# Kernel tuning notes

Measured on AMD Instinct MI355X. Metric: run time of the kernel, lower is better.

The kernel has to match this reference:

```python
import jax, jax.numpy as jnp
import numpy as np

NU, NB, NI = 50000, 20000, 100000
D = 64
NUM_LAYERS = 2
CORE_K = 3
PAD = NI  # padding index for bundle_items
BATCH, NCAND = 2048, 2
MAXDEG = 50
E_UB, E_UI, E_BI = 800000, 1000000, 1200000
N_UB, N_UI, N_BI = NU + NB, NU + NI, NB + NI


def setup_inputs():
    key = jax.random.key(0)
    ks = jax.random.split(key, 24)
    f = jnp.float32
    inp = {
        'users_feature': jax.random.normal(ks[0], (NU, D), f) * 0.1,
        'bundles_feature': jax.random.normal(ks[1], (NB, D), f) * 0.1,
        'items_feature': jax.random.normal(ks[2], (NI, D), f) * 0.1,
        'mlp_core_w1': jax.random.normal(ks[3], (2, 32), f) * 0.1,
        'mlp_core_b1': jnp.zeros((32,), f),
        'mlp_core_w2': jax.random.normal(ks[4], (32, 1), f) * 0.1,
        'mlp_core_b2': jnp.zeros((1,), f),
        'mlp_syn_w1': jax.random.normal(ks[5], (2 * D, D), f) * 0.05,
        'mlp_syn_b1': jnp.zeros((D,), f),
        'mlp_syn_w2': jax.random.normal(ks[6], (D, D), f) * 0.05,
        'mlp_syn_b2': jnp.zeros((D,), f),
        'ub_val': jax.random.uniform(ks[7], (E_UB,), f) * 0.2,
        'ui_val': jax.random.uniform(ks[8], (E_UI,), f) * 0.2,
        'bi_val': jax.random.uniform(ks[9], (E_BI,), f) * 0.2,
        'users': jax.random.randint(ks[10], (BATCH,), 0, NU),
        'bundles': jax.random.randint(ks[11], (BATCH, NCAND), 0, NB),
        'ub_row': jax.random.randint(ks[12], (E_UB,), 0, N_UB, jnp.int32),
        'ub_col': jax.random.randint(ks[13], (E_UB,), 0, N_UB, jnp.int32),
        'ui_row': jax.random.randint(ks[14], (E_UI,), 0, N_UI, jnp.int32),
        'ui_col': jax.random.randint(ks[15], (E_UI,), 0, N_UI, jnp.int32),
        'bi_row': jax.random.randint(ks[16], (E_BI,), 0, N_BI, jnp.int32),
        'bi_col': jax.random.randint(ks[17], (E_BI,), 0, N_BI, jnp.int32),
        'bundle_items': jax.random.randint(ks[18], (NB, MAXDEG), 0, NI + 1),
    }
    return inp


def spmm(row, col, val, x):
    # y = A @ x for COO sparse A: gather source rows, scale, scatter-add to dest rows
    return jax.ops.segment_sum(val[:, None] * x[col], row, num_segments=x.shape[0])


def propagate(row, col, val, feat_a, feat_b):
    f = jnp.concatenate([feat_a, feat_b], axis=0)
    acc = f
    for _ in range(NUM_LAYERS):
        f = spmm(row, col, val, f)
        acc = acc + f
    m = acc / (NUM_LAYERS + 1)  # mean over hop outputs
    return m[:feat_a.shape[0]], m[feat_a.shape[0]:]


def core_fringe_scores(users, bundles, reps, bundle_items,
                       cw1, cb1, cw2, cb2, sw1, sb1, sw2, sb2):
    UB_u, UB_b, UI_u, UI_i, BI_b, BI_i = reps
    B, C = bundles.shape
    users_exp = jnp.repeat(users, C)            # [B*C]
    bundles_flat = bundles.reshape(-1)          # [B*C]
    bbi = bundle_items[bundles_flat]            # [B*C, M]
    mask = bbi != PAD
    zero = jnp.zeros((1, D), UI_i.dtype)
    items_ui = jnp.concatenate([UI_i, zero], 0)[bbi]  # [B*C, M, D]
    items_bi = jnp.concatenate([BI_i, zero], 0)[bbi]
    u_ui = UI_u[users_exp]                      # [B*C, D]
    b_bi = BI_b[bundles_flat]
    r_UI = jnp.einsum('nd,nmd->nm', u_ui, items_ui)
    r_BI = jnp.einsum('nd,nmd->nm', b_bi, items_bi)
    x = jnp.stack([r_UI, r_BI], axis=-1)        # [B*C, M, 2]
    h = jax.nn.relu(x @ cw1 + cb1)              # dropout omitted (eval-mode determinism)
    logits = (h @ cw2 + cb2)[..., 0]
    logits = jnp.where(mask, logits, -jnp.inf)
    pi = jax.nn.softmax(logits, axis=1)
    k = min(CORE_K, bbi.shape[1])
    topv, topi = jax.lax.top_k(pi, k)
    topp = topv / (topv.sum(axis=1, keepdims=True) + 1e-10)
    core_emb = jnp.take_along_axis(items_ui, topi[:, :, None], axis=1)
    h_core = (core_emb * topp[:, :, None]).sum(axis=1)
    n = pi.shape[0]
    is_core = jnp.zeros(pi.shape, bool).at[jnp.arange(n)[:, None], topi].set(True)
    is_fringe = mask & ~is_core
    fr = is_fringe[:, :, None].astype(items_ui.dtype)
    fringe_sum = (items_ui * fr).sum(axis=1)
    fringe_cnt = jnp.maximum(is_fringe.sum(axis=1, keepdims=True).astype(items_ui.dtype), 1.0)
    h_fringe = fringe_sum / fringe_cnt
    syn = jnp.concatenate([h_core, h_fringe], axis=1)
    phi = jax.nn.relu(syn @ sw1 + sb1) @ sw2 + sb2
    hat_e_BI = h_core + phi
    user_final = jnp.concatenate([u_ui, UB_u[users_exp]], axis=1)
    bundle_final = jnp.concatenate([UB_b[bundles_flat], hat_e_BI], axis=1)
    scores = (user_final * bundle_final).sum(axis=1)
    return scores.reshape(B, C)


def reference(users_feature, bundles_feature, items_feature,
              mlp_core_w1, mlp_core_b1, mlp_core_w2, mlp_core_b2,
              mlp_syn_w1, mlp_syn_b1, mlp_syn_w2, mlp_syn_b2,
              ub_val, ui_val, bi_val,
              users, bundles, ub_row, ub_col, ui_row, ui_col,
              bi_row, bi_col, bundle_items):
    UB_u, UB_b = propagate(ub_row, ub_col, ub_val, users_feature, bundles_feature)
    UI_u, UI_i = propagate(ui_row, ui_col, ui_val, users_feature, items_feature)
    BI_b, BI_i = propagate(bi_row, bi_col, bi_val, bundles_feature, items_feature)
    reps = (UB_u, UB_b, UI_u, UI_i, BI_b, BI_i)
    scores = core_fringe_scores(users, bundles, reps, bundle_items,
                                mlp_core_w1, mlp_core_b1, mlp_core_w2, mlp_core_b2,
                                mlp_syn_w1, mlp_syn_b1, mlp_syn_w2, mlp_syn_b2)
    # BPR loss: -log(sigmoid(pos - neg)) == softplus(neg - pos)
    bpr_loss = jnp.mean(jax.nn.softplus(scores[:, 1:] - scores[:, 0:1]))
    return bpr_loss
```

## Files before the change

kernel.cpp:

```cpp
#include <hip/hip_runtime.h>
#include <math.h>

constexpr int D = 64;
constexpr int NU = 50000, NB = 20000, NI = 100000;
constexpr int BATCH = 2048, NCAND = 2, MAXDEG = 50, CORE_K = 3;
constexpr int PAD_IDX = NI;
constexpr int N_UB = NU + NB, N_UI = NU + NI, N_BI = NB + NI;
constexpr int N_TOT = N_UB + N_UI + N_BI;
constexpr int OFF1 = N_UB;
constexpr int OFF2 = N_UB + N_UI;
constexpr int CAP = 48;
constexpr float VAL_SCALE = 16383.0f / 0.2f;
constexpr float VAL_INV   = 0.2f / 16383.0f;

constexpr int GB_BASE = NU;
constexpr int GI_BASE = NU + NB;
constexpr int NGF = NU + NB + NI;

constexpr int BSHIFT = 11;
constexpr int BROWS  = 1 << BSHIFT;
constexpr int NBUCK  = (N_TOT + BROWS - 1) >> BSHIFT;
constexpr int BCAP   = 28672;
constexpr int P1_EPT = 16;
constexpr int P1_TPB = 256;
constexpr int P1_EPB = P1_EPT * P1_TPB;

constexpr int L2_NCB = BATCH * NCAND;
constexpr int L2_SLOTS = 2 * NI + 2 * BATCH + 2 * L2_NCB;
constexpr int S_UBU = 2 * NI;
constexpr int S_UIU = 2 * NI + BATCH;
constexpr int S_UBB = 2 * NI + 2 * BATCH;
constexpr int S_BIB = S_UBB + L2_NCB;

__device__ __forceinline__ float wave_sum64(float v) {
#pragma unroll
    for (int off = 32; off > 0; off >>= 1) v += __shfl_down(v, off);
    return v;
}

__device__ __forceinline__ float bflo(unsigned u) { return __uint_as_float(u << 16); }
__device__ __forceinline__ float bfhi(unsigned u) { return __uint_as_float(u & 0xFFFF0000u); }
__device__ __forceinline__ unsigned short f2bf(float f) {
    unsigned u = __float_as_uint(f);
    u += 0x7FFF + ((u >> 16) & 1);
    return (unsigned short)(u >> 16);
}
__device__ __forceinline__ unsigned pack2(float a, float b) {
    return (unsigned)f2bf(a) | ((unsigned)f2bf(b) << 16);
}
__device__ __forceinline__ float bf1(const unsigned short* p) {
    return __uint_as_float(((unsigned)*p) << 16);
}

__global__ __launch_bounds__(256) void k_bin1(
    const int* __restrict__ r0, const int* __restrict__ c0,
    const float* __restrict__ v0,
    const int* __restrict__ r1, const int* __restrict__ c1,
    const float* __restrict__ v1,
    const int* __restrict__ r2, const int* __restrict__ c2,
    const float* __restrict__ v2,
    int e0, int e1, int e2,
    int* __restrict__ bcnt, uint2* __restrict__ stage) {
    __shared__ int s_hist[NBUCK];
    __shared__ unsigned s_base[NBUCK];
    const int t = threadIdx.x;
    const int etot = e0 + e1 + e2;
    const int i0 = blockIdx.x * P1_EPB + t;
    if (t < NBUCK) s_hist[t] = 0;
    __syncthreads();
    unsigned el[P1_EPT], er[P1_EPT];
#pragma unroll
    for (int k = 0; k < P1_EPT; ++k) {
        int i = i0 + k * P1_TPB;
        if (i < etot) {
            int r, g; float v;
            if (i < e0)           { r = r0[i]; g = c0[i]; v = v0[i]; }
            else if (i < e0 + e1) { int j = i - e0; r = r1[j] + OFF1;
                                    int c = c1[j]; g = (c < NU) ? c : c + NB; v = v1[j]; }
            else                  { int j = i - e0 - e1; r = r2[j] + OFF2;
                                    g = c2[j] + NU; v = v2[j]; }
            unsigned q = (unsigned)fminf(v * VAL_SCALE + 0.5f, 16383.0f);
            el[k] = (q << 18) | (unsigned)g;
            int lo = atomicAdd(&s_hist[r >> BSHIFT], 1);
            er[k] = (unsigned)r | ((unsigned)lo << 19);
        } else {
            er[k] = 0xFFFFFFFFu;
        }
    }
    __syncthreads();
    if (t < NBUCK) s_base[t] = (unsigned)atomicAdd(&bcnt[t], s_hist[t]);
    __syncthreads();
#pragma unroll
    for (int k = 0; k < P1_EPT; ++k) {
        unsigned eh = er[k];
        if (eh == 0xFFFFFFFFu) continue;
        unsigned r = eh & 0x7FFFFu;
        unsigned b = r >> BSHIFT;
        unsigned slot = s_base[b] + (eh >> 19);
        if (slot < (unsigned)BCAP)
            stage[(size_t)b * BCAP + slot] = make_uint2(el[k], r);
    }
}

__global__ __launch_bounds__(1024) void k_bin2(
    const int* __restrict__ bcnt, const uint2* __restrict__ stage,
    int* __restrict__ cnt, unsigned* __restrict__ cv) {
    __shared__ int s_c[BROWS];
    const int b = blockIdx.x;
    const int t = threadIdx.x;
    for (int l = t; l < BROWS; l += 1024) s_c[l] = 0;
    __syncthreads();
    int nb = bcnt[b]; if (nb > BCAP) nb = BCAP;
    const uint2* sp = stage + (size_t)b * BCAP;
    const int rbase = b << BSHIFT;
    for (int i = t; i < nb; i += 1024) {
        uint2 e = sp[i];
        int r = (int)e.y;
        int slot = atomicAdd(&s_c[r - rbase], 1);
        if (slot < CAP) cv[(size_t)r * CAP + slot] = e.x;
    }
    __syncthreads();
    for (int l = t; l < BROWS; l += 1024) {
        int r = rbase + l;
        if (r < N_TOT) cnt[r] = s_c[l];
    }
}

__global__ __launch_bounds__(256) void k_cvt(const float* __restrict__ uf,
                                             const float* __restrict__ bf,
                                             const float* __restrict__ itf,
                                             unsigned short* __restrict__ gt) {
    size_t i = (size_t)blockIdx.x * 256 + threadIdx.x;
    if (i >= (size_t)NGF * 16) return;
    int row = (int)(i >> 4);
    int q = ((int)i & 15) * 4;
    const float* src;
    if (row < GB_BASE)      src = uf  + (size_t)row * D;
    else if (row < GI_BASE) src = bf  + (size_t)(row - GB_BASE) * D;
    else                    src = itf + (size_t)(row - GI_BASE) * D;
    float4 v = *(const float4*)(src + q);
    ushort4 o;
    o.x = f2bf(v.x); o.y = f2bf(v.y); o.z = f2bf(v.z); o.w = f2bf(v.w);
    *(ushort4*)(gt + (size_t)row * D + q) = o;
}

__device__ __forceinline__ void edge_decode(unsigned u, int& col, float& v) {
    col = (int)(u & 0x3FFFFu);
    v = (float)(u >> 18) * VAL_INV;
}

__global__ __launch_bounds__(256) void k_spmm_l1(
    const int* __restrict__ cnt, const unsigned* __restrict__ cv,
    const unsigned short* __restrict__ gt, unsigned short* __restrict__ y1) {
    int r = blockIdx.x * 32 + (threadIdx.x >> 3);
    int t = threadIdx.x & 7;
    if (r >= N_TOT) return;
    int deg = cnt[r]; if (deg > CAP) deg = CAP;
    const unsigned* ce = cv + (size_t)r * CAP;
    float a[8];
#pragma unroll
    for (int k = 0; k < 8; ++k) a[k] = 0.f;
    int j = 0;
    for (; j + 3 < deg; j += 4) {
        int c[4]; float v[4]; uint4 u[4];
#pragma unroll
        for (int k = 0; k < 4; ++k) edge_decode(ce[j + k], c[k], v[k]);
#pragma unroll
        for (int k = 0; k < 4; ++k)
            u[k] = *(const uint4*)(gt + (((size_t)c[k]) << 6) + t * 8);
#pragma unroll
        for (int k = 0; k < 4; ++k) {
            a[0] = fmaf(v[k], bflo(u[k].x), a[0]); a[1] = fmaf(v[k], bfhi(u[k].x), a[1]);
            a[2] = fmaf(v[k], bflo(u[k].y), a[2]); a[3] = fmaf(v[k], bfhi(u[k].y), a[3]);
            a[4] = fmaf(v[k], bflo(u[k].z), a[4]); a[5] = fmaf(v[k], bfhi(u[k].z), a[5]);
            a[6] = fmaf(v[k], bflo(u[k].w), a[6]); a[7] = fmaf(v[k], bfhi(u[k].w), a[7]);
        }
    }
    for (; j < deg; ++j) {
        int c0; float v0;
        edge_decode(ce[j], c0, v0);
        uint4 u0 = *(const uint4*)(gt + (((size_t)c0) << 6) + t * 8);
        a[0] = fmaf(v0, bflo(u0.x), a[0]); a[1] = fmaf(v0, bfhi(u0.x), a[1]);
        a[2] = fmaf(v0, bflo(u0.y), a[2]); a[3] = fmaf(v0, bfhi(u0.y), a[3]);
        a[4] = fmaf(v0, bflo(u0.z), a[4]); a[5] = fmaf(v0, bfhi(u0.z), a[5]);
        a[6] = fmaf(v0, bflo(u0.w), a[6]); a[7] = fmaf(v0, bfhi(u0.w), a[7]);
    }
    uint4 o;
    o.x = pack2(a[0], a[1]); o.y = pack2(a[2], a[3]);
    o.z = pack2(a[4], a[5]); o.w = pack2(a[6], a[7]);
    *(uint4*)(y1 + ((size_t)r << 6) + t * 8) = o;
}

__global__ __launch_bounds__(256) void k_spmm_l2(
    const int* __restrict__ cnt, const unsigned* __restrict__ cv,
    const int* __restrict__ users, const int* __restrict__ bundles,
    const unsigned short* __restrict__ y1, const unsigned short* __restrict__ gt,
    unsigned short* __restrict__ xc) {
    int s = blockIdx.x * 32 + (threadIdx.x >> 3);
    int t = threadIdx.x & 7;
    if (s >= L2_SLOTS) return;
    int r, g, sec;
    if (s < NI)                { r = OFF1 + NU + s;        g = GI_BASE + s;        sec = 1; }
    else if (s < 2 * NI)       { int i = s - NI;
                                 r = OFF2 + NB + i;        g = GI_BASE + i;        sec = 2; }
    else {
        int q = s - 2 * NI;
        if (q < BATCH)            { int u = users[q];             r = u;         g = u;            sec = 0; }
        else if (q < 2 * BATCH)   { int u = users[q - BATCH];     r = OFF1 + u;  g = u;            sec = 1; }
        else if (q < S_BIB - 2 * NI) { int b = bundles[q - 2 * BATCH];
                                    r = NU + b;    g = GB_BASE + b;  sec = 0; }
        else                      { int b = bundles[q - (S_BIB - 2 * NI)];
                                    r = OFF2 + b;  g = GB_BASE + b;  sec = 2; }
    }
    auto y1row = [&](int gg) -> int {
        if (sec == 0) return gg;
        if (sec == 2) return OFF2 - GB_BASE + gg;
        return OFF1 + ((gg < NU) ? gg : gg - NB);
    };
    int deg = cnt[r]; if (deg > CAP) deg = CAP;
    const unsigned* ce = cv + (size_t)r * CAP;
    float a[8];
#pragma unroll
    for (int k = 0; k < 8; ++k) a[k] = 0.f;
    int j = 0;
    for (; j + 3 < deg; j += 4) {
        int c[4]; float v[4]; uint4 u[4];
#pragma unroll
        for (int k = 0; k < 4; ++k) edge_decode(ce[j + k], c[k], v[k]);
#pragma unroll
        for (int k = 0; k < 4; ++k)
            u[k] = *(const uint4*)(y1 + (((size_t)y1row(c[k])) << 6) + t * 8);
#pragma unroll
        for (int k = 0; k < 4; ++k) {
            a[0] = fmaf(v[k], bflo(u[k].x), a[0]); a[1] = fmaf(v[k], bfhi(u[k].x), a[1]);
            a[2] = fmaf(v[k], bflo(u[k].y), a[2]); a[3] = fmaf(v[k], bfhi(u[k].y), a[3]);
            a[4] = fmaf(v[k], bflo(u[k].z), a[4]); a[5] = fmaf(v[k], bfhi(u[k].z), a[5]);
            a[6] = fmaf(v[k], bflo(u[k].w), a[6]); a[7] = fmaf(v[k], bfhi(u[k].w), a[7]);
        }
    }
    for (; j < deg; ++j) {
        int c0; float v0;
        edge_decode(ce[j], c0, v0);
        uint4 u0 = *(const uint4*)(y1 + (((size_t)y1row(c0)) << 6) + t * 8);
        a[0] = fmaf(v0, bflo(u0.x), a[0]); a[1] = fmaf(v0, bfhi(u0.x), a[1]);
        a[2] = fmaf(v0, bflo(u0.y), a[2]); a[3] = fmaf(v0, bfhi(u0.y), a[3]);
        a[4] = fmaf(v0, bflo(u0.z), a[4]); a[5] = fmaf(v0, bfhi(u0.z), a[5]);
        a[6] = fmaf(v0, bflo(u0.w), a[6]); a[7] = fmaf(v0, bfhi(u0.w), a[7]);
    }
    uint4 fx = *(const uint4*)(gt + ((size_t)g << 6) + t * 8);
    uint4 yx = *(const uint4*)(y1 + ((size_t)r << 6) + t * 8);
    constexpr float k3 = 1.0f / 3.0f;
    float o[8];
    o[0] = (bflo(fx.x) + bflo(yx.x) + a[0]) * k3;
    o[1] = (bfhi(fx.x) + bfhi(yx.x) + a[1]) * k3;
    o[2] = (bflo(fx.y) + bflo(yx.y) + a[2]) * k3;
    o[3] = (bfhi(fx.y) + bfhi(yx.y) + a[3]) * k3;
    o[4] = (bflo(fx.z) + bflo(yx.z) + a[4]) * k3;
    o[5] = (bfhi(fx.z) + bfhi(yx.z) + a[5]) * k3;
    o[6] = (bflo(fx.w) + bflo(yx.w) + a[6]) * k3;
    o[7] = (bfhi(fx.w) + bfhi(yx.w) + a[7]) * k3;
    uint4 w;
    w.x = pack2(o[0], o[1]); w.y = pack2(o[2], o[3]);
    w.z = pack2(o[4], o[5]); w.w = pack2(o[6], o[7]);
    *(uint4*)(xc + ((size_t)s << 6) + t * 8) = w;
}

__global__ __launch_bounds__(256) void k_score(
    const int* __restrict__ bundles,
    const int* __restrict__ bundle_items,
    const unsigned short* __restrict__ xc,
    const float* __restrict__ cw1, const float* __restrict__ cb1,
    const float* __restrict__ cw2, const float* __restrict__ cb2,
    const float* __restrict__ sw1, const float* __restrict__ sb1,
    const float* __restrict__ sw2, const float* __restrict__ sb2,
    float* __restrict__ scores) {
    const int t  = threadIdx.x;
    const int wv = t >> 6;
    const int ln = t & 63;
    const int n  = blockIdx.x * 4 + wv;
    const int g8 = ln >> 3;
    const int l8 = ln & 7;
    const int uq = n >> 1;
    const int b = bundles[n];

    __shared__ unsigned sh_it[4][MAXDEG][32];
    __shared__ float sh_r[4][2][MAXDEG];
    __shared__ float sh_syn[4][2 * D];
    __shared__ float sh_h1[4][D];

    int my_idx = (ln < MAXDEG) ? bundle_items[(size_t)b * MAXDEG + ln] : PAD_IDX;
    unsigned long long vmask = __ballot(my_idx != PAD_IDX);

    uint4 ufr = *(const uint4*)(xc + (((size_t)(S_UIU + uq)) << 6) + l8 * 8);
    uint4 bfr = *(const uint4*)(xc + (((size_t)(S_BIB + n)) << 6) + l8 * 8);
    float uf0 = bflo(ufr.x), uf1 = bfhi(ufr.x), uf2 = bflo(ufr.y), uf3 = bfhi(ufr.y);
    float uf4 = bflo(ufr.z), uf5 = bfhi(ufr.z), uf6 = bflo(ufr.w), uf7 = bfhi(ufr.w);
    float bf0 = bflo(bfr.x), bf1_ = bfhi(bfr.x), bf2 = bflo(bfr.y), bf3 = bfhi(bfr.y);
    float bf4 = bflo(bfr.z), bf5 = bfhi(bfr.z), bf6 = bflo(bfr.w), bf7 = bfhi(bfr.w);

    for (int iter = 0; iter < (MAXDEG + 7) / 8; ++iter) {
        int m = iter * 8 + g8;
        if (m >= MAXDEG) continue;
        int it = __shfl(my_idx, m);
        uint4 iu = make_uint4(0, 0, 0, 0);
        float pu = 0.f, pb = 0.f;
        if (it != PAD_IDX) {
            iu = *(const uint4*)(xc + (((size_t)it) << 6) + l8 * 8);
            uint4 ib = *(const uint4*)(xc + (((size_t)(NI + it)) << 6) + l8 * 8);
            pu = uf0 * bflo(iu.x) + uf1 * bfhi(iu.x) + uf2 * bflo(iu.y) + uf3 * bfhi(iu.y)
               + uf4 * bflo(iu.z) + uf5 * bfhi(iu.z) + uf6 * bflo(iu.w) + uf7 * bfhi(iu.w);
            pb = bf0 * bflo(ib.x) + bf1_ * bfhi(ib.x) + bf2 * bflo(ib.y) + bf3 * bfhi(ib.y)
               + bf4 * bflo(ib.z) + bf5 * bfhi(ib.z) + bf6 * bflo(ib.w) + bf7 * bfhi(ib.w);
        }
        *(uint4*)&sh_it[wv][m][l8 * 4] = iu;
#pragma unroll
        for (int off = 4; off > 0; off >>= 1) {
            pu += __shfl_down(pu, off, 8);
            pb += __shfl_down(pb, off, 8);
        }
        if (l8 == 0) { sh_r[wv][0][m] = pu; sh_r[wv][1][m] = pb; }
    }
    __builtin_amdgcn_wave_barrier();

    float logit = -INFINITY;
    if (ln < MAXDEG && my_idx != PAD_IDX) {
        float rU = sh_r[wv][0][ln], rB = sh_r[wv][1][ln];
        float acc = cb2[0];
#pragma unroll
        for (int j = 0; j < 32; ++j) {
            float h = fmaf(rU, cw1[j], fmaf(rB, cw1[32 + j], cb1[j]));
            h = fmaxf(h, 0.f);
            acc = fmaf(h, cw2[j], acc);
        }
        logit = acc;
    }

    float mx = logit;
#pragma unroll
    for (int off = 32; off > 0; off >>= 1) mx = fmaxf(mx, __shfl_xor(mx, off));
    float e = expf(logit - mx);
    float sm = e;
#pragma unroll
    for (int off = 32; off > 0; off >>= 1) sm += __shfl_xor(sm, off);
    float p = e / sm;

    int ti[CORE_K]; float tp[CORE_K];
    float vsel = p;
#pragma unroll
    for (int k = 0; k < CORE_K; ++k) {
        float vv = vsel; int ii = ln;
#pragma unroll
        for (int off = 32; off > 0; off >>= 1) {
            float v2 = __shfl_xor(vv, off);
            int   i2 = __shfl_xor(ii, off);
            if (v2 > vv || (v2 == vv && i2 < ii)) { vv = v2; ii = i2; }
        }
        ti[k] = ii; tp[k] = vv;
        if (ln == ii) vsel = -1.f;
    }
    float tinv = 1.f / (tp[0] + tp[1] + tp[2] + 1e-10f);
    tp[0] *= tinv; tp[1] *= tinv; tp[2] *= tinv;

    int ti0 = ti[0], ti1 = ti[1], ti2 = ti[2];
    const int ui_w = ln >> 1;
    const bool hi = (ln & 1);
    auto feat = [&](int m) -> float {
        unsigned w = sh_it[wv][m][ui_w];
        return hi ? bfhi(w) : bflo(w);
    };
    float hcore = feat(ti0) * tp[0] + feat(ti1) * tp[1] + feat(ti2) * tp[2];
    float fsum = 0.f;
#pragma unroll 10
    for (int m = 0; m < MAXDEG; ++m) fsum += feat(m);
    int fcnt = __popcll(vmask);
#pragma unroll
    for (int k = 0; k < CORE_K; ++k) {
        if ((vmask >> ti[k]) & 1ull) { fsum -= feat(ti[k]); fcnt--; }
    }
    float hfr = fsum / fmaxf((float)fcnt, 1.f);
    sh_syn[wv][ln] = hcore;
    sh_syn[wv][D + ln] = hfr;
    __builtin_amdgcn_wave_barrier();

    float h1 = sb1[ln];
#pragma unroll 8
    for (int k0 = 0; k0 < 32; ++k0) {
        float4 s4 = *(const float4*)&sh_syn[wv][k0 * 4];
        h1 = fmaf(s4.x, sw1[(k0 * 4 + 0) * D + ln], h1);
        h1 = fmaf(s4.y, sw1[(k0 * 4 + 1) * D + ln], h1);
        h1 = fmaf(s4.z, sw1[(k0 * 4 + 2) * D + ln], h1);
        h1 = fmaf(s4.w, sw1[(k0 * 4 + 3) * D + ln], h1);
    }
    sh_h1[wv][ln] = fmaxf(h1, 0.f);
    __builtin_amdgcn_wave_barrier();
    float phi = sb2[ln];
#pragma unroll 8
    for (int k0 = 0; k0 < 16; ++k0) {
        float4 s4 = *(const float4*)&sh_h1[wv][k0 * 4];
        phi = fmaf(s4.x, sw2[(k0 * 4 + 0) * D + ln], phi);
        phi = fmaf(s4.y, sw2[(k0 * 4 + 1) * D + ln], phi);
        phi = fmaf(s4.z, sw2[(k0 * 4 + 2) * D + ln], phi);
        phi = fmaf(s4.w, sw2[(k0 * 4 + 3) * D + ln], phi);
    }

    float hat = hcore + phi;
    float uui = bf1(xc + (((size_t)(S_UIU + uq)) << 6) + ln);
    float ubu = bf1(xc + (((size_t)(S_UBU + uq)) << 6) + ln);
    float ubb = bf1(xc + (((size_t)(S_UBB + n)) << 6) + ln);
    float part = wave_sum64(uui * ubb + ubu * hat);
    if (ln == 0) scores[n] = part;
}

__global__ __launch_bounds__(256) void k_loss(const float* __restrict__ scores,
                                              float* __restrict__ out) {
    __shared__ float red[256];
    float s = 0.f;
    for (int i = threadIdx.x; i < BATCH; i += 256) {
        float x = scores[i * 2 + 1] - scores[i * 2 + 0];
        s += fmaxf(x, 0.f) + log1pf(expf(-fabsf(x)));
    }
    red[threadIdx.x] = s;
    __syncthreads();
    for (int w = 128; w > 0; w >>= 1) {
        if (threadIdx.x < w) red[threadIdx.x] += red[threadIdx.x + w];
        __syncthreads();
    }
    if (threadIdx.x == 0) out[0] = red[0] / (float)BATCH;
}

extern "C" void kernel_launch(void* const* d_in, const int* in_sizes, int n_in,
                              void* d_out, int out_size, void* d_ws, size_t ws_size,
                              hipStream_t stream) {
    const float* users_feature   = (const float*)d_in[0];
    const float* bundles_feature = (const float*)d_in[1];
    const float* items_feature   = (const float*)d_in[2];
    const float* cw1 = (const float*)d_in[3];
    const float* cb1 = (const float*)d_in[4];
    const float* cw2 = (const float*)d_in[5];
    const float* cb2 = (const float*)d_in[6];
    const float* sw1 = (const float*)d_in[7];
    const float* sb1 = (const float*)d_in[8];
    const float* sw2 = (const float*)d_in[9];
    const float* sb2 = (const float*)d_in[10];
    const float* ub_val = (const float*)d_in[11];
    const float* ui_val = (const float*)d_in[12];
    const float* bi_val = (const float*)d_in[13];
    const int* users   = (const int*)d_in[14];
    const int* bundles = (const int*)d_in[15];
    const int* ub_row = (const int*)d_in[16];
    const int* ub_col = (const int*)d_in[17];
    const int* ui_row = (const int*)d_in[18];
    const int* ui_col = (const int*)d_in[19];
    const int* bi_row = (const int*)d_in[20];
    const int* bi_col = (const int*)d_in[21];
    const int* bundle_items = (const int*)d_in[22];
    const int E_UB = in_sizes[11], E_UI = in_sizes[12], E_BI = in_sizes[13];
    const int E_TOT = E_UB + E_UI + E_BI;

    float* ws = (float*)d_ws;
    size_t off = 0;
    unsigned short* gt  = (unsigned short*)(ws + off); off += (size_t)NGF * 32;
    unsigned short* xc  = (unsigned short*)(ws + off); off += (size_t)L2_SLOTS * 32;
    unsigned short* y1b = (unsigned short*)(ws + off); off += (size_t)N_TOT * 32;
    float* scores = ws + off; off += (size_t)BATCH * NCAND;
    int*   cnt    = (int*)(ws + off); off += N_TOT;
    unsigned* cv  = (unsigned*)(ws + off); off += (size_t)N_TOT * CAP;
    int*   bcnt   = (int*)(ws + off); off += NBUCK;
    if (ws_size < off * sizeof(float)) return;

    uint2* stage = (uint2*)y1b;

    hipMemsetAsync(bcnt, 0, NBUCK * sizeof(int), stream);
    k_bin1<<<(E_TOT + P1_EPB - 1) / P1_EPB, P1_TPB, 0, stream>>>(
        ub_row, ub_col, ub_val, ui_row, ui_col, ui_val, bi_row, bi_col, bi_val,
        E_UB, E_UI, E_BI, bcnt, stage);
    k_bin2<<<NBUCK, 1024, 0, stream>>>(bcnt, stage, cnt, cv);

    k_cvt<<<(int)(((size_t)NGF * 16 + 255) / 256), 256, 0, stream>>>(
        users_feature, bundles_feature, items_feature, gt);
    int sb1blocks = (N_TOT + 31) / 32;
    k_spmm_l1<<<sb1blocks, 256, 0, stream>>>(cnt, cv, gt, y1b);
    int sb2blocks = (L2_SLOTS + 31) / 32;
    k_spmm_l2<<<sb2blocks, 256, 0, stream>>>(cnt, cv, users, bundles, y1b, gt, xc);

    k_score<<<(BATCH * NCAND) / 4, 256, 0, stream>>>(
        bundles, bundle_items, xc,
        cw1, cb1, cw2, cb2, sw1, sb1, sw2, sb2, scores);

    k_loss<<<1, 256, 0, stream>>>(scores, (float*)d_out);
}
```

Before: 355.2 us.

## Fuse binning with bf16 conversion, bucket scatter with layer-1 SpMM, and loss into scoring

Runs the feature-to-bf16 conversion as extra blocks of the edge binning kernel. Each row bucket is split into four windows so one 512-thread block scatters its window's edges into the padded CSR and then immediately gathers layer-1 SpMM for those rows. The separate loss kernel is removed: each scoring block computes its softplus terms and accumulates them atomically, and the last block writes the mean. This cuts several launches and lets layer-1 read freshly written edge lists while they are likely still in cache. In exchange every stage bucket is read four times, the bucket capacity is reduced, and the result depends on float atomic ordering.

```diff
diff --git a/kernel.cpp b/kernel.cpp
--- a/kernel.cpp
+++ b/kernel.cpp
@@ -20,10 +20,12 @@
 constexpr int BSHIFT = 11;
 constexpr int BROWS  = 1 << BSHIFT;
 constexpr int NBUCK  = (N_TOT + BROWS - 1) >> BSHIFT;
-constexpr int BCAP   = 28672;
+constexpr int BCAP   = 24576;
 constexpr int P1_EPT = 16;
 constexpr int P1_TPB = 256;
 constexpr int P1_EPB = P1_EPT * P1_TPB;
+constexpr int SPLIT  = 4;
+constexpr int RWIN   = BROWS / SPLIT;
 
 constexpr int L2_NCB = BATCH * NCAND;
 constexpr int L2_SLOTS = 2 * NI + 2 * BATCH + 2 * L2_NCB;
@@ -52,18 +54,70 @@
     return __uint_as_float(((unsigned)*p) << 16);
 }
 
-__global__ __launch_bounds__(256) void k_bin1(
+__device__ __forceinline__ void edge_decode(unsigned u, int& col, float& v) {
+    col = (int)(u & 0x3FFFFu);
+    v = (float)(u >> 18) * VAL_INV;
+}
+
+__device__ __forceinline__ void gather_rows(const unsigned* __restrict__ ce, int deg,
+                                            const unsigned short* __restrict__ src,
+                                            int t8, float a[8]) {
+    int j = 0;
+    for (; j + 3 < deg; j += 4) {
+        int c[4]; float v[4]; uint4 u[4];
+#pragma unroll
+        for (int k = 0; k < 4; ++k) edge_decode(ce[j + k], c[k], v[k]);
+#pragma unroll
+        for (int k = 0; k < 4; ++k)
+            u[k] = *(const uint4*)(src + (((size_t)c[k]) << 6) + t8 * 8);
+#pragma unroll
+        for (int k = 0; k < 4; ++k) {
+            a[0] = fmaf(v[k], bflo(u[k].x), a[0]); a[1] = fmaf(v[k], bfhi(u[k].x), a[1]);
+            a[2] = fmaf(v[k], bflo(u[k].y), a[2]); a[3] = fmaf(v[k], bfhi(u[k].y), a[3]);
+            a[4] = fmaf(v[k], bflo(u[k].z), a[4]); a[5] = fmaf(v[k], bfhi(u[k].z), a[5]);
+            a[6] = fmaf(v[k], bflo(u[k].w), a[6]); a[7] = fmaf(v[k], bfhi(u[k].w), a[7]);
+        }
+    }
+    for (; j < deg; ++j) {
+        int c0; float v0;
+        edge_decode(ce[j], c0, v0);
+        uint4 u0 = *(const uint4*)(src + (((size_t)c0) << 6) + t8 * 8);
+        a[0] = fmaf(v0, bflo(u0.x), a[0]); a[1] = fmaf(v0, bfhi(u0.x), a[1]);
+        a[2] = fmaf(v0, bflo(u0.y), a[2]); a[3] = fmaf(v0, bfhi(u0.y), a[3]);
+        a[4] = fmaf(v0, bflo(u0.z), a[4]); a[5] = fmaf(v0, bfhi(u0.z), a[5]);
+        a[6] = fmaf(v0, bflo(u0.w), a[6]); a[7] = fmaf(v0, bfhi(u0.w), a[7]);
+    }
+}
+
+__global__ __launch_bounds__(256) void k_bin1cvt(
     const int* __restrict__ r0, const int* __restrict__ c0,
     const float* __restrict__ v0,
     const int* __restrict__ r1, const int* __restrict__ c1,
     const float* __restrict__ v1,
     const int* __restrict__ r2, const int* __restrict__ c2,
     const float* __restrict__ v2,
-    int e0, int e1, int e2,
-    int* __restrict__ bcnt, uint2* __restrict__ stage) {
+    int e0, int e1, int e2, int nb1,
+    int* __restrict__ bcnt, uint2* __restrict__ stage,
+    const float* __restrict__ uf, const float* __restrict__ bf,
+    const float* __restrict__ itf, unsigned short* __restrict__ gt) {
+    const int t = threadIdx.x;
+    if ((int)blockIdx.x >= nb1) {
+        size_t i = (size_t)(blockIdx.x - nb1) * 256 + t;
+        if (i >= (size_t)NGF * 16) return;
+        int row = (int)(i >> 4);
+        int q = ((int)i & 15) * 4;
+        const float* src;
+        if (row < GB_BASE)      src = uf  + (size_t)row * D;
+        else if (row < GI_BASE) src = bf  + (size_t)(row - GB_BASE) * D;
+        else                    src = itf + (size_t)(row - GI_BASE) * D;
+        float4 v = *(const float4*)(src + q);
+        ushort4 o;
+        o.x = f2bf(v.x); o.y = f2bf(v.y); o.z = f2bf(v.z); o.w = f2bf(v.w);
+        *(ushort4*)(gt + (size_t)row * D + q) = o;
+        return;
+    }
     __shared__ int s_hist[NBUCK];
     __shared__ unsigned s_base[NBUCK];
-    const int t = threadIdx.x;
     const int etot = e0 + e1 + e2;
     const int i0 = blockIdx.x * P1_EPB + t;
     if (t < NBUCK) s_hist[t] = 0;
@@ -102,93 +156,46 @@
     }
 }
 
-__global__ __launch_bounds__(1024) void k_bin2(
+__global__ __launch_bounds__(512) void k_bin2l1(
     const int* __restrict__ bcnt, const uint2* __restrict__ stage,
-    int* __restrict__ cnt, unsigned* __restrict__ cv) {
-    __shared__ int s_c[BROWS];
-    const int b = blockIdx.x;
-    const int t = threadIdx.x;
-    for (int l = t; l < BROWS; l += 1024) s_c[l] = 0;
+    const unsigned short* __restrict__ gt,
+    int* __restrict__ cnt, unsigned* __restrict__ cv,
+    unsigned short* __restrict__ y1) {
+    __shared__ int s_c[RWIN];
+    const int cb = blockIdx.x >> 2;
+    const int p  = blockIdx.x & 3;
+    const int t  = threadIdx.x;
+    const int rb = (cb << BSHIFT) + p * RWIN;
+    s_c[t] = 0;
     __syncthreads();
-    int nb = bcnt[b]; if (nb > BCAP) nb = BCAP;
-    const uint2* sp = stage + (size_t)b * BCAP;
-    const int rbase = b << BSHIFT;
-    for (int i = t; i < nb; i += 1024) {
+    int nb = bcnt[cb]; if (nb > BCAP) nb = BCAP;
+    const uint2* sp = stage + (size_t)cb * BCAP;
+    for (int i = t; i < nb; i += 512) {
         uint2 e = sp[i];
-        int r = (int)e.y;
-        int slot = atomicAdd(&s_c[r - rbase], 1);
-        if (slot < CAP) cv[(size_t)r * CAP + slot] = e.x;
+        int rl = (int)e.y - rb;
+        if ((unsigned)rl < (unsigned)RWIN) {
+            int slot = atomicAdd(&s_c[rl], 1);
+            if (slot < CAP) cv[(size_t)e.y * CAP + slot] = e.x;
+        }
     }
     __syncthreads();
-    for (int l = t; l < BROWS; l += 1024) {
-        int r = rbase + l;
-        if (r < N_TOT) cnt[r] = s_c[l];
-    }
-}
-
-__global__ __launch_bounds__(256) void k_cvt(const float* __restrict__ uf,
-                                             const float* __restrict__ bf,
-                                             const float* __restrict__ itf,
-                                             unsigned short* __restrict__ gt) {
-    size_t i = (size_t)blockIdx.x * 256 + threadIdx.x;
-    if (i >= (size_t)NGF * 16) return;
-    int row = (int)(i >> 4);
-    int q = ((int)i & 15) * 4;
-    const float* src;
-    if (row < GB_BASE)      src = uf  + (size_t)row * D;
-    else if (row < GI_BASE) src = bf  + (size_t)(row - GB_BASE) * D;
-    else                    src = itf + (size_t)(row - GI_BASE) * D;
-    float4 v = *(const float4*)(src + q);
-    ushort4 o;
-    o.x = f2bf(v.x); o.y = f2bf(v.y); o.z = f2bf(v.z); o.w = f2bf(v.w);
-    *(ushort4*)(gt + (size_t)row * D + q) = o;
-}
-
-__device__ __forceinline__ void edge_decode(unsigned u, int& col, float& v) {
-    col = (int)(u & 0x3FFFFu);
-    v = (float)(u >> 18) * VAL_INV;
-}
-
-__global__ __launch_bounds__(256) void k_spmm_l1(
-    const int* __restrict__ cnt, const unsigned* __restrict__ cv,
-    const unsigned short* __restrict__ gt, unsigned short* __restrict__ y1) {
-    int r = blockIdx.x * 32 + (threadIdx.x >> 3);
-    int t = threadIdx.x & 7;
-    if (r >= N_TOT) return;
-    int deg = cnt[r]; if (deg > CAP) deg = CAP;
-    const unsigned* ce = cv + (size_t)r * CAP;
-    float a[8];
-#pragma unroll
-    for (int k = 0; k < 8; ++k) a[k] = 0.f;
-    int j = 0;
-    for (; j + 3 < deg; j += 4) {
-        int c[4]; float v[4]; uint4 u[4];
-#pragma unroll
-        for (int k = 0; k < 4; ++k) edge_decode(ce[j + k], c[k], v[k]);
-#pragma unroll
-        for (int k = 0; k < 4; ++k)
-            u[k] = *(const uint4*)(gt + (((size_t)c[k]) << 6) + t * 8);
-#pragma unroll
-        for (int k = 0; k < 4; ++k) {
-            a[0] = fmaf(v[k], bflo(u[k].x), a[0]); a[1] = fmaf(v[k], bfhi(u[k].x), a[1]);
-            a[2] = fmaf(v[k], bflo(u[k].y), a[2]); a[3] = fmaf(v[k], bfhi(u[k].y), a[3]);
-            a[4] = fmaf(v[k], bflo(u[k].z), a[4]); a[5] = fmaf(v[k], bfhi(u[k].z), a[5]);
-            a[6] = fmaf(v[k], bflo(u[k].w), a[6]); a[7] = fmaf(v[k], bfhi(u[k].w), a[7]);
-        }
-    }
-    for (; j < deg; ++j) {
-        int c0; float v0;
-        edge_decode(ce[j], c0, v0);
-        uint4 u0 = *(const uint4*)(gt + (((size_t)c0) << 6) + t * 8);
-        a[0] = fmaf(v0, bflo(u0.x), a[0]); a[1] = fmaf(v0, bfhi(u0.x), a[1]);
-        a[2] = fmaf(v0, bflo(u0.y), a[2]); a[3] = fmaf(v0, bfhi(u0.y), a[3]);
-        a[4] = fmaf(v0, bflo(u0.z), a[4]); a[5] = fmaf(v0, bfhi(u0.z), a[5]);
-        a[6] = fmaf(v0, bflo(u0.w), a[6]); a[7] = fmaf(v0, bfhi(u0.w), a[7]);
-    }
-    uint4 o;
-    o.x = pack2(a[0], a[1]); o.y = pack2(a[2], a[3]);
-    o.z = pack2(a[4], a[5]); o.w = pack2(a[6], a[7]);
-    *(uint4*)(y1 + ((size_t)r << 6) + t * 8) = o;
+    if (rb + t < N_TOT) cnt[rb + t] = s_c[t];
+    const int t8 = t & 7;
+#pragma unroll 1
+    for (int pass = 0; pass < 8; ++pass) {
+        int rl = pass * 64 + (t >> 3);
+        int r = rb + rl;
+        if (r >= N_TOT) continue;
+        int deg = s_c[rl]; if (deg > CAP) deg = CAP;
+        float a[8];
+#pragma unroll
+        for (int k = 0; k < 8; ++k) a[k] = 0.f;
+        gather_rows(cv + (size_t)r * CAP, deg, gt, t8, a);
+        uint4 o;
+        o.x = pack2(a[0], a[1]); o.y = pack2(a[2], a[3]);
+        o.z = pack2(a[4], a[5]); o.w = pack2(a[6], a[7]);
+        *(uint4*)(y1 + ((size_t)r << 6) + t8 * 8) = o;
+    }
 }
 
 __global__ __launch_bounds__(256) void k_spmm_l2(
@@ -273,7 +280,8 @@
     const float* __restrict__ cw2, const float* __restrict__ cb2,
     const float* __restrict__ sw1, const float* __restrict__ sb1,
     const float* __restrict__ sw2, const float* __restrict__ sb2,
-    float* __restrict__ scores) {
+    float* __restrict__ accum, unsigned* __restrict__ tick,
+    float* __restrict__ out) {
     const int t  = threadIdx.x;
     const int wv = t >> 6;
     const int ln = t & 63;
@@ -287,6 +295,7 @@
     __shared__ float sh_r[4][2][MAXDEG];
     __shared__ float sh_syn[4][2 * D];
     __shared__ float sh_h1[4][D];
+    __shared__ float sh_sc[4];
 
     int my_idx = (ln < MAXDEG) ? bundle_items[(size_t)b * MAXDEG + ln] : PAD_IDX;
     unsigned long long vmask = __ballot(my_idx != PAD_IDX);
@@ -408,24 +417,23 @@
     float ubu = bf1(xc + (((size_t)(S_UBU + uq)) << 6) + ln);
     float ubb = bf1(xc + (((size_t)(S_UBB + n)) << 6) + ln);
     float part = wave_sum64(uui * ubb + ubu * hat);
-    if (ln == 0) scores[n] = part;
-}
-
-__global__ __launch_bounds__(256) void k_loss(const float* __restrict__ scores,
-                                              float* __restrict__ out) {
-    __shared__ float red[256];
-    float s = 0.f;
-    for (int i = threadIdx.x; i < BATCH; i += 256) {
-        float x = scores[i * 2 + 1] - scores[i * 2 + 0];
-        s += fmaxf(x, 0.f) + log1pf(expf(-fabsf(x)));
-    }
-    red[threadIdx.x] = s;
+    if (ln == 0) sh_sc[wv] = part;
+
     __syncthreads();
-    for (int w = 128; w > 0; w >>= 1) {
-        if (threadIdx.x < w) red[threadIdx.x] += red[threadIdx.x + w];
-        __syncthreads();
-    }
-    if (threadIdx.x == 0) out[0] = red[0] / (float)BATCH;
+    if (t == 0) {
+        float x01 = sh_sc[1] - sh_sc[0];
+        float x23 = sh_sc[3] - sh_sc[2];
+        float spv = fmaxf(x01, 0.f) + log1pf(expf(-fabsf(x01)))
+                  + fmaxf(x23, 0.f) + log1pf(expf(-fabsf(x23)));
+        atomicAdd(accum, spv * (1.0f / (float)BATCH));
+        __threadfence();
+        unsigned old = atomicAdd(tick, 1u);
+        if (old == gridDim.x - 1) {
+            __threadfence();
+            float total = atomicAdd(accum, 0.0f);
+            out[0] = total;
+        }
+    }
 }
 
 extern "C" void kernel_launch(void* const* d_in, const int* in_sizes, int n_in,
@@ -460,32 +468,33 @@
     float* ws = (float*)d_ws;
     size_t off = 0;
     unsigned short* gt  = (unsigned short*)(ws + off); off += (size_t)NGF * 32;
-    unsigned short* xc  = (unsigned short*)(ws + off); off += (size_t)L2_SLOTS * 32;
     unsigned short* y1b = (unsigned short*)(ws + off); off += (size_t)N_TOT * 32;
-    float* scores = ws + off; off += (size_t)BATCH * NCAND;
+    unsigned* cv  = (unsigned*)(ws + off); off += (size_t)N_TOT * CAP;
+    uint2* stage = (uint2*)(ws + off);
+    unsigned short* xc = (unsigned short*)(ws + off);
+    off += (size_t)NBUCK * BCAP * 2;
     int*   cnt    = (int*)(ws + off); off += N_TOT;
-    unsigned* cv  = (unsigned*)(ws + off); off += (size_t)N_TOT * CAP;
     int*   bcnt   = (int*)(ws + off); off += NBUCK;
+    unsigned* tick = (unsigned*)(ws + off); off += 1;
+    float* accum  = (float*)(ws + off); off += 1;
     if (ws_size < off * sizeof(float)) return;
 
-    uint2* stage = (uint2*)y1b;
-
-    hipMemsetAsync(bcnt, 0, NBUCK * sizeof(int), stream);
-    k_bin1<<<(E_TOT + P1_EPB - 1) / P1_EPB, P1_TPB, 0, stream>>>(
+    hipMemsetAsync(bcnt, 0, (NBUCK + 2) * sizeof(int), stream);
+
+    const int nb1 = (E_TOT + P1_EPB - 1) / P1_EPB;
+    const int ncvt = (int)(((size_t)NGF * 16 + 255) / 256);
+    k_bin1cvt<<<nb1 + ncvt, P1_TPB, 0, stream>>>(
         ub_row, ub_col, ub_val, ui_row, ui_col, ui_val, bi_row, bi_col, bi_val,
-        E_UB, E_UI, E_BI, bcnt, stage);
-    k_bin2<<<NBUCK, 1024, 0, stream>>>(bcnt, stage, cnt, cv);
-
-    k_cvt<<<(int)(((size_t)NGF * 16 + 255) / 256), 256, 0, stream>>>(
+        E_UB, E_UI, E_BI, nb1, bcnt, stage,
         users_feature, bundles_feature, items_feature, gt);
-    int sb1blocks = (N_TOT + 31) / 32;
-    k_spmm_l1<<<sb1blocks, 256, 0, stream>>>(cnt, cv, gt, y1b);
-    int sb2blocks = (L2_SLOTS + 31) / 32;
-    k_spmm_l2<<<sb2blocks, 256, 0, stream>>>(cnt, cv, users, bundles, y1b, gt, xc);
+
+    k_bin2l1<<<NBUCK * SPLIT, 512, 0, stream>>>(bcnt, stage, gt, cnt, cv, y1b);
+
+    k_spmm_l2<<<(L2_SLOTS + 31) / 32, 256, 0, stream>>>(
+        cnt, cv, users, bundles, y1b, gt, xc);
 
     k_score<<<(BATCH * NCAND) / 4, 256, 0, stream>>>(
         bundles, bundle_items, xc,
-        cw1, cb1, cw2, cb2, sw1, sb1, sw2, sb2, scores);
-
-    k_loss<<<1, 256, 0, stream>>>(scores, (float*)d_out);
-}
+        cw1, cb1, cw2, cb2, sw1, sb1, sw2, sb2,
+        accum, tick, (float*)d_out);
+}
```

Result: slower. 381.4 us (+7.4%).
